# Kernel tuning notes

Hardware: AMD Instinct MI355X
Metric: run time of the kernel (lower is better)

Reference implementation:

```python
import jax, jax.numpy as jnp
import numpy as np

D, H, L, FF = 512, 8, 6, 2048
EPS = 1e-5


def _ln(x, g, b):
    m = x.mean(-1, keepdims=True)
    v = ((x - m) ** 2).mean(-1, keepdims=True)
    return (x - m) * jax.lax.rsqrt(v + EPS) * g + b


def _mha(qi, ki, vi, w, b):
    # w: [4, D, D] (q, k, v, out), b: [4, D]; weights stored [in, out]
    B, Sq, _ = qi.shape
    Sk = ki.shape[1]
    dk = D // H
    q = (qi @ w[0] + b[0]).reshape(B, Sq, H, dk)
    k = (ki @ w[1] + b[1]).reshape(B, Sk, H, dk)
    v = (vi @ w[2] + b[2]).reshape(B, Sk, H, dk)
    scores = jnp.einsum('bqhd,bkhd->bhqk', q, k) / np.float32(np.sqrt(dk))
    attn = jax.nn.softmax(scores, axis=-1)
    o = jnp.einsum('bhqk,bkhd->bqhd', attn, v).reshape(B, Sq, D)
    return o @ w[3] + b[3]


def setup_inputs() -> dict:
    key = jax.random.key(0)
    ks = jax.random.split(key, 12)
    bs, c, h, w = 4, D, 32, 32
    nq = 100
    s = np.float32(0.02)
    f32 = jnp.float32
    return {
        'src': jax.random.normal(ks[0], (bs, c, h, w), f32),
        'query_embed': jax.random.normal(ks[1], (nq, D), f32),
        'pos_embed': jax.random.normal(ks[2], (bs, c, h, w), f32),
        # encoder params (stacked over L layers)
        'enc_attn_w': jax.random.normal(ks[3], (L, 4, D, D), f32) * s,
        'enc_attn_b': jnp.zeros((L, 4, D), f32),
        'enc_w1': jax.random.normal(ks[4], (L, D, FF), f32) * s,
        'enc_b1': jnp.zeros((L, FF), f32),
        'enc_w2': jax.random.normal(ks[5], (L, FF, D), f32) * s,
        'enc_b2': jnp.zeros((L, D), f32),
        'enc_ln_w': jnp.ones((L, 2, D), f32),
        'enc_ln_b': jnp.zeros((L, 2, D), f32),
        # decoder params
        'dec_sa_w': jax.random.normal(ks[6], (L, 4, D, D), f32) * s,
        'dec_sa_b': jnp.zeros((L, 4, D), f32),
        'dec_ca_w': jax.random.normal(ks[7], (L, 4, D, D), f32) * s,
        'dec_ca_b': jnp.zeros((L, 4, D), f32),
        'dec_w1': jax.random.normal(ks[8], (L, D, FF), f32) * s,
        'dec_b1': jnp.zeros((L, FF), f32),
        'dec_w2': jax.random.normal(ks[9], (L, FF, D), f32) * s,
        'dec_b2': jnp.zeros((L, D), f32),
        'dec_ln_w': jnp.ones((L, 3, D), f32),
        'dec_ln_b': jnp.zeros((L, 3, D), f32),
    }


def reference(src, query_embed, pos_embed,
              enc_attn_w, enc_attn_b, enc_w1, enc_b1, enc_w2, enc_b2,
              enc_ln_w, enc_ln_b,
              dec_sa_w, dec_sa_b, dec_ca_w, dec_ca_b,
              dec_w1, dec_b1, dec_w2, dec_b2, dec_ln_w, dec_ln_b):
    bs, c, h, w = src.shape
    x = src.reshape(bs, c, h * w).transpose(0, 2, 1)        # [B, HW, D]
    pos = pos_embed.reshape(bs, c, h * w).transpose(0, 2, 1)  # [B, HW, D]
    qe = jnp.broadcast_to(query_embed[None], (bs,) + query_embed.shape)  # [B, NQ, D]

    def enc_step(mem, p):
        aw, ab, w1, b1, w2, b2, lnw, lnb = p
        t = mem + pos  # original re-adds pos_embed every encoder layer
        t = _ln(t + _mha(t, t, t, aw, ab), lnw[0], lnb[0])
        f = jax.nn.relu(t @ w1 + b1) @ w2 + b2
        t = _ln(t + f, lnw[1], lnb[1])
        return t, None

    memory, _ = jax.lax.scan(
        enc_step, x,
        (enc_attn_w, enc_attn_b, enc_w1, enc_b1, enc_w2, enc_b2, enc_ln_w, enc_ln_b))

    mem_in = memory + pos

    def dec_step(out, p):
        saw, sab, caw, cab, w1, b1, w2, b2, lnw, lnb = p
        t = out + qe  # original re-adds query_embed every decoder layer
        t = _ln(t + _mha(t, t, t, saw, sab), lnw[0], lnb[0])
        t = _ln(t + _mha(t, mem_in, mem_in, caw, cab), lnw[1], lnb[1])
        f = jax.nn.relu(t @ w1 + b1) @ w2 + b2
        t = _ln(t + f, lnw[2], lnb[2])
        return t, None

    tgt = jnp.zeros_like(qe)
    output, _ = jax.lax.scan(
        dec_step, tgt,
        (dec_sa_w, dec_sa_b, dec_ca_w, dec_ca_b, dec_w1, dec_b1, dec_w2, dec_b2,
         dec_ln_w, dec_ln_b))
    return output, memory
```

## Files before the change

kernel.cpp:

```cpp
#include <hip/hip_runtime.h>
#include <math.h>


typedef unsigned short bfu;
typedef unsigned int u32;
typedef __bf16 bf8v __attribute__((ext_vector_type(8)));
typedef float f32x4 __attribute__((ext_vector_type(4)));

__device__ inline bfu f2bf(float f) {
  union { float f; u32 u; } v; v.f = f;
  u32 u = v.u;
  u32 r = (u + 0x7fffu + ((u >> 16) & 1u)) >> 16;
  return (bfu)r;
}
__device__ inline float bflo(u32 u) { return __uint_as_float(u << 16); }

typedef const __attribute__((address_space(1))) u32 gas_t;
typedef __attribute__((address_space(3))) u32 las_t;
__device__ __forceinline__ void gl16(const void* g, void* l) {
  __builtin_amdgcn_global_load_lds((gas_t*)g, (las_t*)l, 16, 0, 0);
}

__global__ __launch_bounds__(256) void k_transpose(const float* __restrict__ in,
                                                   float* __restrict__ out) {
  __shared__ float tile[32][33];
  int b = blockIdx.z;
  int c0 = blockIdx.x * 32, s0 = blockIdx.y * 32;
  int tx = threadIdx.x, ty = threadIdx.y;
  for (int i = ty; i < 32; i += 8)
    tile[i][tx] = in[((size_t)(b * 512 + c0 + i)) * 1024 + s0 + tx];
  __syncthreads();
  for (int i = ty; i < 32; i += 8)
    out[((size_t)(b * 1024 + s0 + i)) * 512 + c0 + tx] = tile[tx][i];
}

__global__ __launch_bounds__(256) void k_wt(const float* __restrict__ src,
                                            bfu* __restrict__ dst,
                                            int K, int N, int nj, int lstride) {
  __shared__ bfu tile[32][33];
  int g = blockIdx.z;
  int l = g / nj, j = g - l * nj;
  const float* s = src + ((size_t)l * lstride + j) * (size_t)K * N;
  bfu* d = dst + (size_t)g * (size_t)K * N;
  int n0 = blockIdx.x * 32, k0 = blockIdx.y * 32;
  int tx = threadIdx.x, ty = threadIdx.y;
  for (int i = ty; i < 32; i += 8)
    tile[i][tx] = f2bf(s[(size_t)(k0 + i) * N + n0 + tx]);
  __syncthreads();
  for (int i = ty; i < 32; i += 8)
    d[(size_t)(n0 + i) * K + k0 + tx] = tile[tx][i];
}

__global__ void k_add_dual(const float* __restrict__ a, const float* __restrict__ b,
                           float* __restrict__ of, bfu* __restrict__ ob, int n4) {
  int i = blockIdx.x * blockDim.x + threadIdx.x;
  if (i >= n4) return;
  float4 x = ((const float4*)a)[i];
  float4 y = ((const float4*)b)[i];
  float4 r = make_float4(x.x + y.x, x.y + y.y, x.z + y.z, x.w + y.w);
  ((float4*)of)[i] = r;
  ((ushort4*)ob)[i] = make_ushort4(f2bf(r.x), f2bf(r.y), f2bf(r.z), f2bf(r.w));
}

__global__ void k_qe0(const float* __restrict__ qe, float* __restrict__ of,
                      bfu* __restrict__ ob) {
  int i = blockIdx.x * blockDim.x + threadIdx.x;
  if (i >= 51200) return;
  int row = i >> 7;
  int q = row % 100;
  int c4 = i & 127;
  float4 y = ((const float4*)qe)[q * 128 + c4];
  ((float4*)of)[i] = y;
  ((ushort4*)ob)[i] = make_ushort4(f2bf(y.x), f2bf(y.y), f2bf(y.z), f2bf(y.w));
}

__global__ __launch_bounds__(256) void k_ln_red(const float* __restrict__ A,
                                                const float* __restrict__ P,
                                                int nsplit, size_t pz,
                                                const float* __restrict__ bias,
                                                const float* __restrict__ g,
                                                const float* __restrict__ be,
                                                float* __restrict__ of,
                                                bfu* __restrict__ ob,
                                                const float* __restrict__ add2,
                                                int qe_mode,
                                                float* __restrict__ of2,
                                                bfu* __restrict__ ob2,
                                                int rows) {
  int row = blockIdx.x * 4 + (threadIdx.x >> 6);
  int lane = threadIdx.x & 63;
  if (row >= rows) return;
  const float* pa = A + (size_t)row * 512;
  float v[8];
  float s = 0.f, s2 = 0.f;
#pragma unroll
  for (int j = 0; j < 8; ++j) {
    int c = lane + j * 64;
    float x = pa[c] + bias[c];
    for (int z = 0; z < nsplit; ++z) x += P[z * pz + (size_t)row * 512 + c];
    v[j] = x; s += x; s2 += x * x;
  }
#pragma unroll
  for (int off = 32; off > 0; off >>= 1) {
    s += __shfl_xor(s, off);
    s2 += __shfl_xor(s2, off);
  }
  float mean = s * (1.f / 512.f);
  float var = s2 * (1.f / 512.f) - mean * mean;
  float r = rsqrtf(var + 1e-5f);
  int arow = qe_mode ? (row % 100) : row;
#pragma unroll
  for (int j = 0; j < 8; ++j) {
    int c = lane + j * 64;
    float o = (v[j] - mean) * r * g[c] + be[c];
    if (of) of[(size_t)row * 512 + c] = o;
    if (ob) ob[(size_t)row * 512 + c] = f2bf(o);
    if (add2) {
      float o2 = o + add2[(size_t)arow * 512 + c];
      if (of2) of2[(size_t)row * 512 + c] = o2;
      if (ob2) ob2[(size_t)row * 512 + c] = f2bf(o2);
    }
  }
}

__global__ __launch_bounds__(256) void k_gemm_bf(const bfu* __restrict__ A,
                                                 const bfu* __restrict__ Wt,
                                                 const float* __restrict__ bias,
                                                 bfu* __restrict__ C,
                                                 int M, int N, int K, int relu,
                                                 size_t wtz, size_t cz, int bz) {
  __shared__ bfu As[2][128][64];
  __shared__ bfu Bs[2][128][64];
  int z = blockIdx.z;
  Wt += (size_t)z * wtz; C += (size_t)z * cz; bias += z * bz;
  int bm = blockIdx.y * 128, bn = blockIdx.x * 128;
  int t = threadIdx.x;
  int wave = t >> 6, lane = t & 63;
  int wm = wave >> 1, wn = wave & 1;
  int l15 = lane & 15, l4 = lane >> 4;
  f32x4 acc[4][4];
  f32x4 zz = {0.f, 0.f, 0.f, 0.f};
#pragma unroll
  for (int mi = 0; mi < 4; ++mi)
#pragma unroll
    for (int ni = 0; ni < 4; ++ni) acc[mi][ni] = zz;

  auto stage = [&](int buf, int k0) {
#pragma unroll
    for (int i = 0; i < 4; ++i) {
      int c = t + i * 256;
      int row = c >> 3, kg = c & 7;
      int sc = kg ^ (row & 7);
      if (bm + row < M)
        gl16(A + (size_t)(bm + row) * K + k0 + sc * 8, &As[buf][row][kg * 8]);
      gl16(Wt + (size_t)(bn + row) * K + k0 + sc * 8, &Bs[buf][row][kg * 8]);
    }
  };
  stage(0, 0);
  int cur = 0;
  for (int k0 = 0; k0 < K; k0 += 64) {
    __syncthreads();
    if (k0 + 64 < K) stage(cur ^ 1, k0 + 64);
#pragma unroll
    for (int kc = 0; kc < 2; ++kc) {
      bf8v av[4], bv[4];
#pragma unroll
      for (int mi = 0; mi < 4; ++mi) {
        int row = wm * 64 + mi * 16 + l15;
        av[mi] = *(const bf8v*)&As[cur][row][((kc * 4 + l4) ^ (row & 7)) * 8];
      }
#pragma unroll
      for (int ni = 0; ni < 4; ++ni) {
        int row = wn * 64 + ni * 16 + l15;
        bv[ni] = *(const bf8v*)&Bs[cur][row][((kc * 4 + l4) ^ (row & 7)) * 8];
      }
#pragma unroll
      for (int mi = 0; mi < 4; ++mi)
#pragma unroll
        for (int ni = 0; ni < 4; ++ni)
          acc[mi][ni] = __builtin_amdgcn_mfma_f32_16x16x32_bf16(av[mi], bv[ni],
                                                                acc[mi][ni], 0, 0, 0);
    }
    cur ^= 1;
  }

#pragma unroll
  for (int mi = 0; mi < 4; ++mi) {
    int row0 = bm + wm * 64 + mi * 16 + l4 * 4;
#pragma unroll
    for (int ni = 0; ni < 4; ++ni) {
      int col = bn + wn * 64 + ni * 16 + l15;
      float bb = bias[col];
#pragma unroll
      for (int r = 0; r < 4; ++r) {
        int row = row0 + r;
        if (row < M) {
          float v = acc[mi][ni][r] + bb;
          if (relu) v = fmaxf(v, 0.f);
          C[(size_t)row * N + col] = f2bf(v);
        }
      }
    }
  }
}

__global__ __launch_bounds__(256) void k_gemm_sk(const bfu* __restrict__ A,
                                                 const bfu* __restrict__ Wt,
                                                 float* __restrict__ Pf,
                                                 int M, int N, int K, int ksplit) {
  __shared__ bfu As[2][128][64];
  __shared__ bfu Bs[2][128][64];
  int z = blockIdx.z;
  int Kc = K / ksplit;
  int kbeg = z * Kc;
  Pf += (size_t)z * M * N;
  int bm = blockIdx.y * 128, bn = blockIdx.x * 128;
  int t = threadIdx.x;
  int wave = t >> 6, lane = t & 63;
  int wm = wave >> 1, wn = wave & 1;
  int l15 = lane & 15, l4 = lane >> 4;
  f32x4 acc[4][4];
  f32x4 zz = {0.f, 0.f, 0.f, 0.f};
#pragma unroll
  for (int mi = 0; mi < 4; ++mi)
#pragma unroll
    for (int ni = 0; ni < 4; ++ni) acc[mi][ni] = zz;

  auto stage = [&](int buf, int k0) {
#pragma unroll
    for (int i = 0; i < 4; ++i) {
      int c = t + i * 256;
      int row = c >> 3, kg = c & 7;
      int sc = kg ^ (row & 7);
      if (bm + row < M)
        gl16(A + (size_t)(bm + row) * K + k0 + sc * 8, &As[buf][row][kg * 8]);
      gl16(Wt + (size_t)(bn + row) * K + k0 + sc * 8, &Bs[buf][row][kg * 8]);
    }
  };
  stage(0, kbeg);
  int cur = 0;
  for (int k0 = kbeg; k0 < kbeg + Kc; k0 += 64) {
    __syncthreads();
    if (k0 + 64 < kbeg + Kc) stage(cur ^ 1, k0 + 64);
#pragma unroll
    for (int kc = 0; kc < 2; ++kc) {
      bf8v av[4], bv[4];
#pragma unroll
      for (int mi = 0; mi < 4; ++mi) {
        int row = wm * 64 + mi * 16 + l15;
        av[mi] = *(const bf8v*)&As[cur][row][((kc * 4 + l4) ^ (row & 7)) * 8];
      }
#pragma unroll
      for (int ni = 0; ni < 4; ++ni) {
        int row = wn * 64 + ni * 16 + l15;
        bv[ni] = *(const bf8v*)&Bs[cur][row][((kc * 4 + l4) ^ (row & 7)) * 8];
      }
#pragma unroll
      for (int mi = 0; mi < 4; ++mi)
#pragma unroll
        for (int ni = 0; ni < 4; ++ni)
          acc[mi][ni] = __builtin_amdgcn_mfma_f32_16x16x32_bf16(av[mi], bv[ni],
                                                                acc[mi][ni], 0, 0, 0);
    }
    cur ^= 1;
  }

#pragma unroll
  for (int mi = 0; mi < 4; ++mi) {
    int row0 = bm + wm * 64 + mi * 16 + l4 * 4;
#pragma unroll
    for (int ni = 0; ni < 4; ++ni) {
      int col = bn + wn * 64 + ni * 16 + l15;
#pragma unroll
      for (int r = 0; r < 4; ++r) {
        int row = row0 + r;
        if (row < M) Pf[(size_t)row * N + col] = acc[mi][ni][r];
      }
    }
  }
}

__global__ __launch_bounds__(256) void k_attn_mfma(const bfu* __restrict__ Q, int qs,
                                                   const bfu* __restrict__ Km,
                                                   const bfu* __restrict__ Vm, int kvs,
                                                   bfu* __restrict__ O,
                                                   int Sq, int Sk) {
  __shared__ bfu Ks[128][72];
  __shared__ bfu Vt[64][136];
  __shared__ bfu Sm[4][16][136];
  const float scale = 0.125f;
  int b = blockIdx.z, h = blockIdx.y;
  int q0 = blockIdx.x * 64;
  int t = threadIdx.x;
  int wave = t >> 6, lane = t & 63;
  int l15 = lane & 15, l4 = lane >> 4;
  int hoff = h * 64;

  uint4 uq0 = {0u, 0u, 0u, 0u}, uq1 = {0u, 0u, 0u, 0u};
  {
    int qrow = q0 + wave * 16 + l15;
    if (qrow < Sq) {
      const bfu* qp = Q + (size_t)(b * Sq + qrow) * qs + hoff + l4 * 8;
      uq0 = *(const uint4*)qp;
      uq1 = *(const uint4*)(qp + 32);
    }
  }
  bf8v qf0 = *(bf8v*)&uq0, qf1 = *(bf8v*)&uq1;

  float m_[4] = {-1e30f, -1e30f, -1e30f, -1e30f};
  float l_[4] = {0.f, 0.f, 0.f, 0.f};
  f32x4 oacc[4];
  f32x4 zz = {0.f, 0.f, 0.f, 0.f};
#pragma unroll
  for (int n = 0; n < 4; ++n) oacc[n] = zz;

  uint4 ruk[4], ruv[4];
  const uint4 uz = {0u, 0u, 0u, 0u};
  auto load_kv = [&](int k0) {
#pragma unroll
    for (int i = 0; i < 4; ++i) {
      int e = t + i * 256;
      int rk = e >> 3, cg = e & 7;
      ruk[i] = uz;
      if (k0 + rk < Sk)
        ruk[i] = *(const uint4*)(Km + (size_t)(b * Sk + k0 + rk) * kvs + hoff + cg * 8);
      int kv = e & 127, dg = e >> 7;
      ruv[i] = uz;
      if (k0 + kv < Sk)
        ruv[i] = *(const uint4*)(Vm + (size_t)(b * Sk + k0 + kv) * kvs + hoff + dg * 8);
    }
  };
  load_kv(0);

  for (int k0 = 0; k0 < Sk; k0 += 128) {
#pragma unroll
    for (int i = 0; i < 4; ++i) {
      int e = t + i * 256;
      int rk = e >> 3, cg = e & 7;
      *(uint4*)&Ks[rk][cg * 8] = ruk[i];
      int kv = e & 127, dg = e >> 7;
      bfu vv[8];
      *(uint4*)vv = ruv[i];
#pragma unroll
      for (int j = 0; j < 8; ++j) Vt[dg * 8 + j][kv] = vv[j];
    }
    __syncthreads();
    if (k0 + 128 < Sk) load_kv(k0 + 128);

    f32x4 s4[8];
    __builtin_amdgcn_s_setprio(1);
#pragma unroll
    for (int tt = 0; tt < 8; ++tt) {
      bf8v kf0 = *(const bf8v*)&Ks[tt * 16 + l15][l4 * 8];
      bf8v kf1 = *(const bf8v*)&Ks[tt * 16 + l15][32 + l4 * 8];
      f32x4 a = zz;
      a = __builtin_amdgcn_mfma_f32_16x16x32_bf16(qf0, kf0, a, 0, 0, 0);
      a = __builtin_amdgcn_mfma_f32_16x16x32_bf16(qf1, kf1, a, 0, 0, 0);
      s4[tt] = a;
    }
    __builtin_amdgcn_s_setprio(0);

    float f_[4];
#pragma unroll
    for (int r = 0; r < 4; ++r) {
      float sv[8];
      float mx = -1e30f;
#pragma unroll
      for (int tt = 0; tt < 8; ++tt) {
        float s = s4[tt][r] * scale;
        s = (k0 + tt * 16 + l15 < Sk) ? s : -1e30f;
        sv[tt] = s;
        mx = fmaxf(mx, s);
      }
#pragma unroll
      for (int off = 1; off < 16; off <<= 1) mx = fmaxf(mx, __shfl_xor(mx, off));
      float nm = fmaxf(m_[r], mx);
      float f = __expf(m_[r] - nm);
      float ps = 0.f;
#pragma unroll
      for (int tt = 0; tt < 8; ++tt) {
        float p = __expf(sv[tt] - nm);
        ps += p;
        Sm[wave][l4 * 4 + r][tt * 16 + l15] = f2bf(p);
      }
#pragma unroll
      for (int off = 1; off < 16; off <<= 1) ps += __shfl_xor(ps, off);
      l_[r] = l_[r] * f + ps;
      m_[r] = nm;
      f_[r] = f;
    }
#pragma unroll
    for (int n = 0; n < 4; ++n)
#pragma unroll
      for (int r = 0; r < 4; ++r) oacc[n][r] *= f_[r];

    __builtin_amdgcn_s_setprio(1);
#pragma unroll
    for (int h2 = 0; h2 < 2; ++h2) {
      bf8v p0 = *(const bf8v*)&Sm[wave][l15][h2 * 64 + l4 * 8];
      bf8v p1 = *(const bf8v*)&Sm[wave][l15][h2 * 64 + 32 + l4 * 8];
#pragma unroll
      for (int n = 0; n < 4; ++n) {
        bf8v v0 = *(const bf8v*)&Vt[n * 16 + l15][h2 * 64 + l4 * 8];
        bf8v v1 = *(const bf8v*)&Vt[n * 16 + l15][h2 * 64 + 32 + l4 * 8];
        oacc[n] = __builtin_amdgcn_mfma_f32_16x16x32_bf16(p0, v0, oacc[n], 0, 0, 0);
        oacc[n] = __builtin_amdgcn_mfma_f32_16x16x32_bf16(p1, v1, oacc[n], 0, 0, 0);
      }
    }
    __builtin_amdgcn_s_setprio(0);
    __syncthreads();
  }

#pragma unroll
  for (int r = 0; r < 4; ++r) {
    int row = q0 + wave * 16 + l4 * 4 + r;
    if (row < Sq) {
      float inv = 1.f / l_[r];
#pragma unroll
      for (int n = 0; n < 4; ++n)
        O[(size_t)(b * Sq + row) * 512 + hoff + n * 16 + l15] = f2bf(oacc[n][r] * inv);
    }
  }
}


extern "C" void kernel_launch(void* const* d_in, const int* in_sizes, int n_in,
                              void* d_out, int out_size, void* d_ws, size_t ws_size,
                              hipStream_t stream) {
  const float* src         = (const float*)d_in[0];
  const float* query_embed = (const float*)d_in[1];
  const float* pos_embed   = (const float*)d_in[2];
  const float* enc_attn_w  = (const float*)d_in[3];
  const float* enc_attn_b  = (const float*)d_in[4];
  const float* enc_w1      = (const float*)d_in[5];
  const float* enc_b1      = (const float*)d_in[6];
  const float* enc_w2      = (const float*)d_in[7];
  const float* enc_b2      = (const float*)d_in[8];
  const float* enc_ln_w    = (const float*)d_in[9];
  const float* enc_ln_b    = (const float*)d_in[10];
  const float* dec_sa_w    = (const float*)d_in[11];
  const float* dec_sa_b    = (const float*)d_in[12];
  const float* dec_ca_w    = (const float*)d_in[13];
  const float* dec_ca_b    = (const float*)d_in[14];
  const float* dec_w1      = (const float*)d_in[15];
  const float* dec_b1      = (const float*)d_in[16];
  const float* dec_w2      = (const float*)d_in[17];
  const float* dec_b2      = (const float*)d_in[18];
  const float* dec_ln_w    = (const float*)d_in[19];
  const float* dec_ln_b    = (const float*)d_in[20];
  float* out = (float*)d_out;

  const size_t ENC = 4UL * 1024 * 512;
  const size_t DEC = 4UL * 100 * 512;
  const size_t MAT = 512UL * 512;

  float* p = (float*)d_ws;
  float* x    = p; p += ENC;
  float* pos  = p; p += ENC;
  float* t1   = p; p += ENC;
  float* t2   = p; p += ENC;
  float* t3   = p; p += DEC;
  float* Pf   = p; p += 4 * ENC;

  bfu* bp = (bfu*)p;
  bfu* t1b    = bp; bp += ENC;
  bfu* t2b    = bp; bp += ENC;
  bfu* t3b    = bp; bp += DEC;
  bfu* qkvb   = bp; bp += 4096UL * 1536;
  bfu* aob    = bp; bp += ENC;
  bfu* hbb    = bp; bp += 4096UL * 2048;
  bfu* meminb = bp; bp += ENC;
  bfu* ckvb   = bp; bp += 6UL * 4096 * 1024;
  bfu* enc_qkv_t = bp; bp += 18 * MAT;
  bfu* enc_out_t = bp; bp += 6 * MAT;
  bfu* enc_w1t   = bp; bp += 6UL * 512 * 2048;
  bfu* enc_w2t   = bp; bp += 6UL * 2048 * 512;
  bfu* dsa_qkv_t = bp; bp += 18 * MAT;
  bfu* dsa_out_t = bp; bp += 6 * MAT;
  bfu* dca_q_t   = bp; bp += 6 * MAT;
  bfu* dca_kv_t  = bp; bp += 12 * MAT;
  bfu* dca_out_t = bp; bp += 6 * MAT;
  bfu* dw1t      = bp; bp += 6UL * 512 * 2048;
  bfu* dw2t      = bp; bp += 6UL * 2048 * 512;

  dim3 tb(32, 8);
  k_transpose<<<dim3(16, 32, 4), tb, 0, stream>>>(src, x);
  k_transpose<<<dim3(16, 32, 4), tb, 0, stream>>>(pos_embed, pos);

  k_wt<<<dim3(16, 16, 18), tb, 0, stream>>>(enc_attn_w,            enc_qkv_t, 512, 512, 3, 4);
  k_wt<<<dim3(16, 16, 6),  tb, 0, stream>>>(enc_attn_w + 3 * MAT,  enc_out_t, 512, 512, 1, 4);
  k_wt<<<dim3(64, 16, 6),  tb, 0, stream>>>(enc_w1,                enc_w1t,   512, 2048, 1, 1);
  k_wt<<<dim3(16, 64, 6),  tb, 0, stream>>>(enc_w2,                enc_w2t,   2048, 512, 1, 1);
  k_wt<<<dim3(16, 16, 18), tb, 0, stream>>>(dec_sa_w,              dsa_qkv_t, 512, 512, 3, 4);
  k_wt<<<dim3(16, 16, 6),  tb, 0, stream>>>(dec_sa_w + 3 * MAT,    dsa_out_t, 512, 512, 1, 4);
  k_wt<<<dim3(16, 16, 6),  tb, 0, stream>>>(dec_ca_w,              dca_q_t,   512, 512, 1, 4);
  k_wt<<<dim3(16, 16, 12), tb, 0, stream>>>(dec_ca_w + 1 * MAT,    dca_kv_t,  512, 512, 2, 4);
  k_wt<<<dim3(16, 16, 6),  tb, 0, stream>>>(dec_ca_w + 3 * MAT,    dca_out_t, 512, 512, 1, 4);
  k_wt<<<dim3(64, 16, 6),  tb, 0, stream>>>(dec_w1,                dw1t,      512, 2048, 1, 1);
  k_wt<<<dim3(16, 64, 6),  tb, 0, stream>>>(dec_w2,                dw2t,      2048, 512, 1, 1);

  k_add_dual<<<2048, 256, 0, stream>>>(x, pos, t1, t1b, (int)(ENC / 4));
  for (int l = 0; l < 6; ++l) {
    const float* ab = enc_attn_b + (size_t)l * 2048;
    k_gemm_bf<<<dim3(12, 32), 256, 0, stream>>>(t1b, enc_qkv_t + (size_t)l * 3 * MAT, ab,
                                                qkvb, 4096, 1536, 512, 0, 0, 0, 0);
    k_attn_mfma<<<dim3(16, 8, 4), 256, 0, stream>>>(qkvb, 1536, qkvb + 512, qkvb + 1024, 1536,
                                                    aob, 1024, 1024);
    k_gemm_sk<<<dim3(4, 32, 2), 256, 0, stream>>>(aob, enc_out_t + (size_t)l * MAT, Pf,
                                                  4096, 512, 512, 2);
    k_ln_red<<<1024, 256, 0, stream>>>(t1, Pf, 2, ENC, ab + 1536,
                                       enc_ln_w + (size_t)(l * 2 + 0) * 512,
                                       enc_ln_b + (size_t)(l * 2 + 0) * 512,
                                       t2, t2b, (const float*)nullptr, 0,
                                       (float*)nullptr, (bfu*)nullptr, 4096);
    k_gemm_bf<<<dim3(16, 32), 256, 0, stream>>>(t2b, enc_w1t + (size_t)l * 512 * 2048,
                                                enc_b1 + (size_t)l * 2048, hbb,
                                                4096, 2048, 512, 1, 0, 0, 0);
    k_gemm_sk<<<dim3(4, 32, 4), 256, 0, stream>>>(hbb, enc_w2t + (size_t)l * 2048 * 512, Pf,
                                                  4096, 512, 2048, 4);
    if (l < 5) {
      k_ln_red<<<1024, 256, 0, stream>>>(t2, Pf, 4, ENC, enc_b2 + (size_t)l * 512,
                                         enc_ln_w + (size_t)(l * 2 + 1) * 512,
                                         enc_ln_b + (size_t)(l * 2 + 1) * 512,
                                         (float*)nullptr, (bfu*)nullptr,
                                         pos, 0, t1, t1b, 4096);
    } else {
      k_ln_red<<<1024, 256, 0, stream>>>(t2, Pf, 4, ENC, enc_b2 + (size_t)l * 512,
                                         enc_ln_w + (size_t)(l * 2 + 1) * 512,
                                         enc_ln_b + (size_t)(l * 2 + 1) * 512,
                                         out + DEC, (bfu*)nullptr,
                                         pos, 0, (float*)nullptr, meminb, 4096);
    }
  }

  k_gemm_bf<<<dim3(8, 32, 6), 256, 0, stream>>>(meminb, dca_kv_t, dec_ca_b + 512,
                                                ckvb, 4096, 1024, 512, 0,
                                                2 * MAT, 4096UL * 1024, 2048);

  k_qe0<<<200, 256, 0, stream>>>(query_embed, t1, t1b);
  for (int l = 0; l < 6; ++l) {
    const float* sb = dec_sa_b + (size_t)l * 2048;
    const float* cb = dec_ca_b + (size_t)l * 2048;
    k_gemm_bf<<<dim3(12, 4), 256, 0, stream>>>(t1b, dsa_qkv_t + (size_t)l * 3 * MAT, sb,
                                               qkvb, 400, 1536, 512, 0, 0, 0, 0);
    k_attn_mfma<<<dim3(2, 8, 4), 256, 0, stream>>>(qkvb, 1536, qkvb + 512, qkvb + 1024, 1536,
                                                   aob, 100, 100);
    k_gemm_sk<<<dim3(4, 4, 2), 256, 0, stream>>>(aob, dsa_out_t + (size_t)l * MAT, Pf,
                                                 400, 512, 512, 2);
    k_ln_red<<<100, 256, 0, stream>>>(t1, Pf, 2, 400UL * 512, sb + 1536,
                                      dec_ln_w + (size_t)(l * 3 + 0) * 512,
                                      dec_ln_b + (size_t)(l * 3 + 0) * 512,
                                      t2, t2b, (const float*)nullptr, 0,
                                      (float*)nullptr, (bfu*)nullptr, 400);
    k_gemm_bf<<<dim3(4, 4), 256, 0, stream>>>(t2b, dca_q_t + (size_t)l * MAT, cb,
                                              qkvb, 400, 512, 512, 0, 0, 0, 0);
    k_attn_mfma<<<dim3(2, 8, 4), 256, 0, stream>>>(qkvb, 512,
                                                   ckvb + (size_t)l * 4096 * 1024,
                                                   ckvb + (size_t)l * 4096 * 1024 + 512, 1024,
                                                   aob, 100, 1024);
    k_gemm_sk<<<dim3(4, 4, 2), 256, 0, stream>>>(aob, dca_out_t + (size_t)l * MAT, Pf,
                                                 400, 512, 512, 2);
    k_ln_red<<<100, 256, 0, stream>>>(t2, Pf, 2, 400UL * 512, cb + 1536,
                                      dec_ln_w + (size_t)(l * 3 + 1) * 512,
                                      dec_ln_b + (size_t)(l * 3 + 1) * 512,
                                      t3, t3b, (const float*)nullptr, 0,
                                      (float*)nullptr, (bfu*)nullptr, 400);
    k_gemm_bf<<<dim3(16, 4), 256, 0, stream>>>(t3b, dw1t + (size_t)l * 512 * 2048,
                                               dec_b1 + (size_t)l * 2048, hbb,
                                               400, 2048, 512, 1, 0, 0, 0);
    k_gemm_sk<<<dim3(4, 4, 4), 256, 0, stream>>>(hbb, dw2t + (size_t)l * 2048 * 512, Pf,
                                                 400, 512, 2048, 4);
    if (l < 5) {
      k_ln_red<<<100, 256, 0, stream>>>(t3, Pf, 4, 400UL * 512, dec_b2 + (size_t)l * 512,
                                        dec_ln_w + (size_t)(l * 3 + 2) * 512,
                                        dec_ln_b + (size_t)(l * 3 + 2) * 512,
                                        (float*)nullptr, (bfu*)nullptr,
                                        query_embed, 1, t1, t1b, 400);
    } else {
      k_ln_red<<<100, 256, 0, stream>>>(t3, Pf, 4, 400UL * 512, dec_b2 + (size_t)l * 512,
                                        dec_ln_w + (size_t)(l * 3 + 2) * 512,
                                        dec_ln_b + (size_t)(l * 3 + 2) * 512,
                                        out, (bfu*)nullptr,
                                        (const float*)nullptr, 0,
                                        (float*)nullptr, (bfu*)nullptr, 400);
    }
  }
}
```

Baseline: 1.997 ms.

## Fuse output-projection and FFN2 GEMMs with residual LayerNorm epilogue

Replaces the split-K GEMM plus separate LayerNorm reduction kernels with a single GEMM kernel that computes full 512-wide rows per block (32 rows x 512 cols) and applies bias, residual add, and LayerNorm in the epilogue through a cross-wave shared-memory reduction. This drops the fp32 partial-sum buffer and its write/read traffic, and removes one kernel launch per sublayer. Weight transposes are merged into fewer launches and the two input transposes into one. The trade-off is far fewer blocks (128 for the encoder, 13 for the decoder) with no split-K, so the decoder GEMMs, especially the K=2048 FFN2, run on very few CUs.

Result: slower. 2.615 ms (+31.0%).

```diff
diff --git a/kernel.cpp b/kernel.cpp
--- a/kernel.cpp
+++ b/kernel.cpp
@@ -21,26 +21,30 @@
   __builtin_amdgcn_global_load_lds((gas_t*)g, (las_t*)l, 16, 0, 0);
 }
 
-__global__ __launch_bounds__(256) void k_transpose(const float* __restrict__ in,
-                                                   float* __restrict__ out) {
+__global__ __launch_bounds__(256) void k_transpose2(const float* __restrict__ s0,
+                                                    const float* __restrict__ s1,
+                                                    float* __restrict__ d0,
+                                                    float* __restrict__ d1) {
   __shared__ float tile[32][33];
-  int b = blockIdx.z;
-  int c0 = blockIdx.x * 32, s0 = blockIdx.y * 32;
+  int zz = blockIdx.z;
+  const float* in = (zz < 4) ? s0 : s1;
+  float* out = (zz < 4) ? d0 : d1;
+  int b = zz & 3;
+  int c0 = blockIdx.x * 32, s0i = blockIdx.y * 32;
   int tx = threadIdx.x, ty = threadIdx.y;
   for (int i = ty; i < 32; i += 8)
-    tile[i][tx] = in[((size_t)(b * 512 + c0 + i)) * 1024 + s0 + tx];
+    tile[i][tx] = in[((size_t)(b * 512 + c0 + i)) * 1024 + s0i + tx];
   __syncthreads();
   for (int i = ty; i < 32; i += 8)
-    out[((size_t)(b * 1024 + s0 + i)) * 512 + c0 + tx] = tile[tx][i];
+    out[((size_t)(b * 1024 + s0i + i)) * 512 + c0 + tx] = tile[tx][i];
 }
 
 __global__ __launch_bounds__(256) void k_wt(const float* __restrict__ src,
                                             bfu* __restrict__ dst,
-                                            int K, int N, int nj, int lstride) {
+                                            int K, int N) {
   __shared__ bfu tile[32][33];
   int g = blockIdx.z;
-  int l = g / nj, j = g - l * nj;
-  const float* s = src + ((size_t)l * lstride + j) * (size_t)K * N;
+  const float* s = src + (size_t)g * (size_t)K * N;
   bfu* d = dst + (size_t)g * (size_t)K * N;
   int n0 = blockIdx.x * 32, k0 = blockIdx.y * 32;
   int tx = threadIdx.x, ty = threadIdx.y;
@@ -72,55 +76,6 @@
   float4 y = ((const float4*)qe)[q * 128 + c4];
   ((float4*)of)[i] = y;
   ((ushort4*)ob)[i] = make_ushort4(f2bf(y.x), f2bf(y.y), f2bf(y.z), f2bf(y.w));
-}
-
-__global__ __launch_bounds__(256) void k_ln_red(const float* __restrict__ A,
-                                                const float* __restrict__ P,
-                                                int nsplit, size_t pz,
-                                                const float* __restrict__ bias,
-                                                const float* __restrict__ g,
-                                                const float* __restrict__ be,
-                                                float* __restrict__ of,
-                                                bfu* __restrict__ ob,
-                                                const float* __restrict__ add2,
-                                                int qe_mode,
-                                                float* __restrict__ of2,
-                                                bfu* __restrict__ ob2,
-                                                int rows) {
-  int row = blockIdx.x * 4 + (threadIdx.x >> 6);
-  int lane = threadIdx.x & 63;
-  if (row >= rows) return;
-  const float* pa = A + (size_t)row * 512;
-  float v[8];
-  float s = 0.f, s2 = 0.f;
-#pragma unroll
-  for (int j = 0; j < 8; ++j) {
-    int c = lane + j * 64;
-    float x = pa[c] + bias[c];
-    for (int z = 0; z < nsplit; ++z) x += P[z * pz + (size_t)row * 512 + c];
-    v[j] = x; s += x; s2 += x * x;
-  }
-#pragma unroll
-  for (int off = 32; off > 0; off >>= 1) {
-    s += __shfl_xor(s, off);
-    s2 += __shfl_xor(s2, off);
-  }
-  float mean = s * (1.f / 512.f);
-  float var = s2 * (1.f / 512.f) - mean * mean;
-  float r = rsqrtf(var + 1e-5f);
-  int arow = qe_mode ? (row % 100) : row;
-#pragma unroll
-  for (int j = 0; j < 8; ++j) {
-    int c = lane + j * 64;
-    float o = (v[j] - mean) * r * g[c] + be[c];
-    if (of) of[(size_t)row * 512 + c] = o;
-    if (ob) ob[(size_t)row * 512 + c] = f2bf(o);
-    if (add2) {
-      float o2 = o + add2[(size_t)arow * 512 + c];
-      if (of2) of2[(size_t)row * 512 + c] = o2;
-      if (ob2) ob2[(size_t)row * 512 + c] = f2bf(o2);
-    }
-  }
 }
 
 __global__ __launch_bounds__(256) void k_gemm_bf(const bfu* __restrict__ A,
@@ -204,80 +159,125 @@
   }
 }
 
-__global__ __launch_bounds__(256) void k_gemm_sk(const bfu* __restrict__ A,
+__global__ __launch_bounds__(256) void k_gemm_ln(const bfu* __restrict__ A,
                                                  const bfu* __restrict__ Wt,
-                                                 float* __restrict__ Pf,
-                                                 int M, int N, int K, int ksplit) {
-  __shared__ bfu As[2][128][64];
-  __shared__ bfu Bs[2][128][64];
-  int z = blockIdx.z;
-  int Kc = K / ksplit;
-  int kbeg = z * Kc;
-  Pf += (size_t)z * M * N;
-  int bm = blockIdx.y * 128, bn = blockIdx.x * 128;
+                                                 const float* __restrict__ bias,
+                                                 const float* __restrict__ R,
+                                                 const float* __restrict__ g,
+                                                 const float* __restrict__ be,
+                                                 float* __restrict__ of,
+                                                 bfu* __restrict__ ob,
+                                                 const float* __restrict__ add2,
+                                                 int qe_mode,
+                                                 float* __restrict__ of2,
+                                                 bfu* __restrict__ ob2,
+                                                 int M, int K) {
+  __shared__ bfu As[2][32][32];
+  __shared__ bfu Bs[2][512][32];
+  __shared__ float red[32][4][2];
+  int bm = blockIdx.x * 32;
   int t = threadIdx.x;
   int wave = t >> 6, lane = t & 63;
-  int wm = wave >> 1, wn = wave & 1;
   int l15 = lane & 15, l4 = lane >> 4;
-  f32x4 acc[4][4];
+  f32x4 acc[2][8];
   f32x4 zz = {0.f, 0.f, 0.f, 0.f};
 #pragma unroll
-  for (int mi = 0; mi < 4; ++mi)
-#pragma unroll
-    for (int ni = 0; ni < 4; ++ni) acc[mi][ni] = zz;
+  for (int mt = 0; mt < 2; ++mt)
+#pragma unroll
+    for (int nt = 0; nt < 8; ++nt) acc[mt][nt] = zz;
 
   auto stage = [&](int buf, int k0) {
 #pragma unroll
-    for (int i = 0; i < 4; ++i) {
-      int c = t + i * 256;
-      int row = c >> 3, kg = c & 7;
-      int sc = kg ^ (row & 7);
-      if (bm + row < M)
-        gl16(A + (size_t)(bm + row) * K + k0 + sc * 8, &As[buf][row][kg * 8]);
-      gl16(Wt + (size_t)(bn + row) * K + k0 + sc * 8, &Bs[buf][row][kg * 8]);
+    for (int i = 0; i < 8; ++i) {
+      int cb = t + i * 256;
+      int r = cb >> 2, p = cb & 3;
+      int gp = p ^ ((r >> 2) & 3);
+      gl16(Wt + (size_t)r * K + k0 + gp * 8, &Bs[buf][r][p * 8]);
+    }
+    if (t < 128) {
+      int r = t >> 2, p = t & 3;
+      int gp = p ^ ((r >> 2) & 3);
+      if (bm + r < M)
+        gl16(A + (size_t)(bm + r) * K + k0 + gp * 8, &As[buf][r][p * 8]);
     }
   };
-  stage(0, kbeg);
+  stage(0, 0);
   int cur = 0;
-  for (int k0 = kbeg; k0 < kbeg + Kc; k0 += 64) {
+  for (int k0 = 0; k0 < K; k0 += 32) {
     __syncthreads();
-    if (k0 + 64 < kbeg + Kc) stage(cur ^ 1, k0 + 64);
-#pragma unroll
-    for (int kc = 0; kc < 2; ++kc) {
-      bf8v av[4], bv[4];
-#pragma unroll
-      for (int mi = 0; mi < 4; ++mi) {
-        int row = wm * 64 + mi * 16 + l15;
-        av[mi] = *(const bf8v*)&As[cur][row][((kc * 4 + l4) ^ (row & 7)) * 8];
-      }
-#pragma unroll
-      for (int ni = 0; ni < 4; ++ni) {
-        int row = wn * 64 + ni * 16 + l15;
-        bv[ni] = *(const bf8v*)&Bs[cur][row][((kc * 4 + l4) ^ (row & 7)) * 8];
-      }
-#pragma unroll
-      for (int mi = 0; mi < 4; ++mi)
-#pragma unroll
-        for (int ni = 0; ni < 4; ++ni)
-          acc[mi][ni] = __builtin_amdgcn_mfma_f32_16x16x32_bf16(av[mi], bv[ni],
-                                                                acc[mi][ni], 0, 0, 0);
+    if (k0 + 32 < K) stage(cur ^ 1, k0 + 32);
+    bf8v av[2];
+#pragma unroll
+    for (int mt = 0; mt < 2; ++mt) {
+      int r = mt * 16 + l15;
+      av[mt] = *(const bf8v*)&As[cur][r][(l4 ^ ((r >> 2) & 3)) * 8];
+    }
+#pragma unroll
+    for (int nt = 0; nt < 8; ++nt) {
+      int rb = wave * 128 + nt * 16 + l15;
+      bf8v bv = *(const bf8v*)&Bs[cur][rb][(l4 ^ ((rb >> 2) & 3)) * 8];
+      acc[0][nt] = __builtin_amdgcn_mfma_f32_16x16x32_bf16(av[0], bv, acc[0][nt], 0, 0, 0);
+      acc[1][nt] = __builtin_amdgcn_mfma_f32_16x16x32_bf16(av[1], bv, acc[1][nt], 0, 0, 0);
     }
     cur ^= 1;
   }
 
-#pragma unroll
-  for (int mi = 0; mi < 4; ++mi) {
-    int row0 = bm + wm * 64 + mi * 16 + l4 * 4;
-#pragma unroll
-    for (int ni = 0; ni < 4; ++ni) {
-      int col = bn + wn * 64 + ni * 16 + l15;
-#pragma unroll
-      for (int r = 0; r < 4; ++r) {
-        int row = row0 + r;
-        if (row < M) Pf[(size_t)row * N + col] = acc[mi][ni][r];
-      }
-    }
-  }
+  float bs[8], gg[8], bb[8];
+#pragma unroll
+  for (int nt = 0; nt < 8; ++nt) {
+    int gc = wave * 128 + nt * 16 + l15;
+    bs[nt] = bias[gc]; gg[nt] = g[gc]; bb[nt] = be[gc];
+  }
+#pragma unroll
+  for (int mt = 0; mt < 2; ++mt)
+#pragma unroll
+    for (int rr = 0; rr < 4; ++rr) {
+      int row32 = mt * 16 + l4 * 4 + rr;
+      int gm = bm + row32;
+      float s = 0.f, s2 = 0.f;
+      if (gm < M) {
+#pragma unroll
+        for (int nt = 0; nt < 8; ++nt) {
+          int gc = wave * 128 + nt * 16 + l15;
+          float v = acc[mt][nt][rr] + bs[nt] + R[(size_t)gm * 512 + gc];
+          acc[mt][nt][rr] = v;
+          s += v; s2 += v * v;
+        }
+      }
+#pragma unroll
+      for (int off = 1; off < 16; off <<= 1) {
+        s += __shfl_xor(s, off);
+        s2 += __shfl_xor(s2, off);
+      }
+      if (l15 == 0) { red[row32][wave][0] = s; red[row32][wave][1] = s2; }
+    }
+  __syncthreads();
+#pragma unroll
+  for (int mt = 0; mt < 2; ++mt)
+#pragma unroll
+    for (int rr = 0; rr < 4; ++rr) {
+      int row32 = mt * 16 + l4 * 4 + rr;
+      int gm = bm + row32;
+      if (gm >= M) continue;
+      float s = red[row32][0][0] + red[row32][1][0] + red[row32][2][0] + red[row32][3][0];
+      float s2 = red[row32][0][1] + red[row32][1][1] + red[row32][2][1] + red[row32][3][1];
+      float mean = s * (1.f / 512.f);
+      float var = s2 * (1.f / 512.f) - mean * mean;
+      float rs = rsqrtf(var + 1e-5f);
+      int arow = qe_mode ? (gm % 100) : gm;
+#pragma unroll
+      for (int nt = 0; nt < 8; ++nt) {
+        int gc = wave * 128 + nt * 16 + l15;
+        float o = (acc[mt][nt][rr] - mean) * rs * gg[nt] + bb[nt];
+        if (of) of[(size_t)gm * 512 + gc] = o;
+        if (ob) ob[(size_t)gm * 512 + gc] = f2bf(o);
+        if (add2) {
+          float o2 = o + add2[(size_t)arow * 512 + gc];
+          if (of2) of2[(size_t)gm * 512 + gc] = o2;
+          if (ob2) ob2[(size_t)gm * 512 + gc] = f2bf(o2);
+        }
+      }
+    }
 }
 
 __global__ __launch_bounds__(256) void k_attn_mfma(const bfu* __restrict__ Q, int qs,
@@ -460,7 +460,6 @@
   float* t1   = p; p += ENC;
   float* t2   = p; p += ENC;
   float* t3   = p; p += DEC;
-  float* Pf   = p; p += 4 * ENC;
 
   bfu* bp = (bfu*)p;
   bfu* t1b    = bp; bp += ENC;
@@ -471,118 +470,106 @@
   bfu* hbb    = bp; bp += 4096UL * 2048;
   bfu* meminb = bp; bp += ENC;
   bfu* ckvb   = bp; bp += 6UL * 4096 * 1024;
-  bfu* enc_qkv_t = bp; bp += 18 * MAT;
-  bfu* enc_out_t = bp; bp += 6 * MAT;
+  bfu* enc_att_t = bp; bp += 24 * MAT;
   bfu* enc_w1t   = bp; bp += 6UL * 512 * 2048;
   bfu* enc_w2t   = bp; bp += 6UL * 2048 * 512;
-  bfu* dsa_qkv_t = bp; bp += 18 * MAT;
-  bfu* dsa_out_t = bp; bp += 6 * MAT;
-  bfu* dca_q_t   = bp; bp += 6 * MAT;
-  bfu* dca_kv_t  = bp; bp += 12 * MAT;
-  bfu* dca_out_t = bp; bp += 6 * MAT;
+  bfu* dsa_t     = bp; bp += 24 * MAT;
+  bfu* dca_t     = bp; bp += 24 * MAT;
   bfu* dw1t      = bp; bp += 6UL * 512 * 2048;
   bfu* dw2t      = bp; bp += 6UL * 2048 * 512;
 
   dim3 tb(32, 8);
-  k_transpose<<<dim3(16, 32, 4), tb, 0, stream>>>(src, x);
-  k_transpose<<<dim3(16, 32, 4), tb, 0, stream>>>(pos_embed, pos);
-
-  k_wt<<<dim3(16, 16, 18), tb, 0, stream>>>(enc_attn_w,            enc_qkv_t, 512, 512, 3, 4);
-  k_wt<<<dim3(16, 16, 6),  tb, 0, stream>>>(enc_attn_w + 3 * MAT,  enc_out_t, 512, 512, 1, 4);
-  k_wt<<<dim3(64, 16, 6),  tb, 0, stream>>>(enc_w1,                enc_w1t,   512, 2048, 1, 1);
-  k_wt<<<dim3(16, 64, 6),  tb, 0, stream>>>(enc_w2,                enc_w2t,   2048, 512, 1, 1);
-  k_wt<<<dim3(16, 16, 18), tb, 0, stream>>>(dec_sa_w,              dsa_qkv_t, 512, 512, 3, 4);
-  k_wt<<<dim3(16, 16, 6),  tb, 0, stream>>>(dec_sa_w + 3 * MAT,    dsa_out_t, 512, 512, 1, 4);
-  k_wt<<<dim3(16, 16, 6),  tb, 0, stream>>>(dec_ca_w,              dca_q_t,   512, 512, 1, 4);
-  k_wt<<<dim3(16, 16, 12), tb, 0, stream>>>(dec_ca_w + 1 * MAT,    dca_kv_t,  512, 512, 2, 4);
-  k_wt<<<dim3(16, 16, 6),  tb, 0, stream>>>(dec_ca_w + 3 * MAT,    dca_out_t, 512, 512, 1, 4);
-  k_wt<<<dim3(64, 16, 6),  tb, 0, stream>>>(dec_w1,                dw1t,      512, 2048, 1, 1);
-  k_wt<<<dim3(16, 64, 6),  tb, 0, stream>>>(dec_w2,                dw2t,      2048, 512, 1, 1);
+  k_transpose2<<<dim3(16, 32, 8), tb, 0, stream>>>(src, pos_embed, x, pos);
+
+  k_wt<<<dim3(16, 16, 24), tb, 0, stream>>>(enc_attn_w, enc_att_t, 512, 512);
+  k_wt<<<dim3(64, 16, 6),  tb, 0, stream>>>(enc_w1,     enc_w1t,   512, 2048);
+  k_wt<<<dim3(16, 64, 6),  tb, 0, stream>>>(enc_w2,     enc_w2t,   2048, 512);
+  k_wt<<<dim3(16, 16, 24), tb, 0, stream>>>(dec_sa_w,   dsa_t,     512, 512);
+  k_wt<<<dim3(16, 16, 24), tb, 0, stream>>>(dec_ca_w,   dca_t,     512, 512);
+  k_wt<<<dim3(64, 16, 6),  tb, 0, stream>>>(dec_w1,     dw1t,      512, 2048);
+  k_wt<<<dim3(16, 64, 6),  tb, 0, stream>>>(dec_w2,     dw2t,      2048, 512);
 
   k_add_dual<<<2048, 256, 0, stream>>>(x, pos, t1, t1b, (int)(ENC / 4));
   for (int l = 0; l < 6; ++l) {
+    const bfu* awt = enc_att_t + (size_t)l * 4 * MAT;
     const float* ab = enc_attn_b + (size_t)l * 2048;
-    k_gemm_bf<<<dim3(12, 32), 256, 0, stream>>>(t1b, enc_qkv_t + (size_t)l * 3 * MAT, ab,
+    k_gemm_bf<<<dim3(12, 32), 256, 0, stream>>>(t1b, awt, ab,
                                                 qkvb, 4096, 1536, 512, 0, 0, 0, 0);
     k_attn_mfma<<<dim3(16, 8, 4), 256, 0, stream>>>(qkvb, 1536, qkvb + 512, qkvb + 1024, 1536,
                                                     aob, 1024, 1024);
-    k_gemm_sk<<<dim3(4, 32, 2), 256, 0, stream>>>(aob, enc_out_t + (size_t)l * MAT, Pf,
-                                                  4096, 512, 512, 2);
-    k_ln_red<<<1024, 256, 0, stream>>>(t1, Pf, 2, ENC, ab + 1536,
+    k_gemm_ln<<<128, 256, 0, stream>>>(aob, awt + 3 * MAT, ab + 1536, t1,
                                        enc_ln_w + (size_t)(l * 2 + 0) * 512,
                                        enc_ln_b + (size_t)(l * 2 + 0) * 512,
                                        t2, t2b, (const float*)nullptr, 0,
-                                       (float*)nullptr, (bfu*)nullptr, 4096);
+                                       (float*)nullptr, (bfu*)nullptr, 4096, 512);
     k_gemm_bf<<<dim3(16, 32), 256, 0, stream>>>(t2b, enc_w1t + (size_t)l * 512 * 2048,
                                                 enc_b1 + (size_t)l * 2048, hbb,
                                                 4096, 2048, 512, 1, 0, 0, 0);
-    k_gemm_sk<<<dim3(4, 32, 4), 256, 0, stream>>>(hbb, enc_w2t + (size_t)l * 2048 * 512, Pf,
-                                                  4096, 512, 2048, 4);
     if (l < 5) {
-      k_ln_red<<<1024, 256, 0, stream>>>(t2, Pf, 4, ENC, enc_b2 + (size_t)l * 512,
+      k_gemm_ln<<<128, 256, 0, stream>>>(hbb, enc_w2t + (size_t)l * 2048 * 512,
+                                         enc_b2 + (size_t)l * 512, t2,
                                          enc_ln_w + (size_t)(l * 2 + 1) * 512,
                                          enc_ln_b + (size_t)(l * 2 + 1) * 512,
                                          (float*)nullptr, (bfu*)nullptr,
-                                         pos, 0, t1, t1b, 4096);
+                                         pos, 0, t1, t1b, 4096, 2048);
     } else {
-      k_ln_red<<<1024, 256, 0, stream>>>(t2, Pf, 4, ENC, enc_b2 + (size_t)l * 512,
+      k_gemm_ln<<<128, 256, 0, stream>>>(hbb, enc_w2t + (size_t)l * 2048 * 512,
+                                         enc_b2 + (size_t)l * 512, t2,
                                          enc_ln_w + (size_t)(l * 2 + 1) * 512,
                                          enc_ln_b + (size_t)(l * 2 + 1) * 512,
                                          out + DEC, (bfu*)nullptr,
-                                         pos, 0, (float*)nullptr, meminb, 4096);
-    }
-  }
-
-  k_gemm_bf<<<dim3(8, 32, 6), 256, 0, stream>>>(meminb, dca_kv_t, dec_ca_b + 512,
+                                         pos, 0, (float*)nullptr, meminb, 4096, 2048);
+    }
+  }
+
+  k_gemm_bf<<<dim3(8, 32, 6), 256, 0, stream>>>(meminb, dca_t + MAT, dec_ca_b + 512,
                                                 ckvb, 4096, 1024, 512, 0,
-                                                2 * MAT, 4096UL * 1024, 2048);
+                                                4 * MAT, 4096UL * 1024, 2048);
 
   k_qe0<<<200, 256, 0, stream>>>(query_embed, t1, t1b);
   for (int l = 0; l < 6; ++l) {
+    const bfu* swt = dsa_t + (size_t)l * 4 * MAT;
+    const bfu* cwt = dca_t + (size_t)l * 4 * MAT;
     const float* sb = dec_sa_b + (size_t)l * 2048;
     const float* cb = dec_ca_b + (size_t)l * 2048;
-    k_gemm_bf<<<dim3(12, 4), 256, 0, stream>>>(t1b, dsa_qkv_t + (size_t)l * 3 * MAT, sb,
+    k_gemm_bf<<<dim3(12, 4), 256, 0, stream>>>(t1b, swt, sb,
                                                qkvb, 400, 1536, 512, 0, 0, 0, 0);
     k_attn_mfma<<<dim3(2, 8, 4), 256, 0, stream>>>(qkvb, 1536, qkvb + 512, qkvb + 1024, 1536,
                                                    aob, 100, 100);
-    k_gemm_sk<<<dim3(4, 4, 2), 256, 0, stream>>>(aob, dsa_out_t + (size_t)l * MAT, Pf,
-                                                 400, 512, 512, 2);
-    k_ln_red<<<100, 256, 0, stream>>>(t1, Pf, 2, 400UL * 512, sb + 1536,
+    k_gemm_ln<<<13, 256, 0, stream>>>(aob, swt + 3 * MAT, sb + 1536, t1,
                                       dec_ln_w + (size_t)(l * 3 + 0) * 512,
                                       dec_ln_b + (size_t)(l * 3 + 0) * 512,
                                       t2, t2b, (const float*)nullptr, 0,
-                                      (float*)nullptr, (bfu*)nullptr, 400);
-    k_gemm_bf<<<dim3(4, 4), 256, 0, stream>>>(t2b, dca_q_t + (size_t)l * MAT, cb,
+                                      (float*)nullptr, (bfu*)nullptr, 400, 512);
+    k_gemm_bf<<<dim3(4, 4), 256, 0, stream>>>(t2b, cwt, cb,
                                               qkvb, 400, 512, 512, 0, 0, 0, 0);
     k_attn_mfma<<<dim3(2, 8, 4), 256, 0, stream>>>(qkvb, 512,
                                                    ckvb + (size_t)l * 4096 * 1024,
                                                    ckvb + (size_t)l * 4096 * 1024 + 512, 1024,
                                                    aob, 100, 1024);
-    k_gemm_sk<<<dim3(4, 4, 2), 256, 0, stream>>>(aob, dca_out_t + (size_t)l * MAT, Pf,
-                                                 400, 512, 512, 2);
-    k_ln_red<<<100, 256, 0, stream>>>(t2, Pf, 2, 400UL * 512, cb + 1536,
+    k_gemm_ln<<<13, 256, 0, stream>>>(aob, cwt + 3 * MAT, cb + 1536, t2,
                                       dec_ln_w + (size_t)(l * 3 + 1) * 512,
                                       dec_ln_b + (size_t)(l * 3 + 1) * 512,
                                       t3, t3b, (const float*)nullptr, 0,
-                                      (float*)nullptr, (bfu*)nullptr, 400);
+                                      (float*)nullptr, (bfu*)nullptr, 400, 512);
     k_gemm_bf<<<dim3(16, 4), 256, 0, stream>>>(t3b, dw1t + (size_t)l * 512 * 2048,
                                                dec_b1 + (size_t)l * 2048, hbb,
                                                400, 2048, 512, 1, 0, 0, 0);
-    k_gemm_sk<<<dim3(4, 4, 4), 256, 0, stream>>>(hbb, dw2t + (size_t)l * 2048 * 512, Pf,
-                                                 400, 512, 2048, 4);
     if (l < 5) {
-      k_ln_red<<<100, 256, 0, stream>>>(t3, Pf, 4, 400UL * 512, dec_b2 + (size_t)l * 512,
+      k_gemm_ln<<<13, 256, 0, stream>>>(hbb, dw2t + (size_t)l * 2048 * 512,
+                                        dec_b2 + (size_t)l * 512, t3,
                                         dec_ln_w + (size_t)(l * 3 + 2) * 512,
                                         dec_ln_b + (size_t)(l * 3 + 2) * 512,
                                         (float*)nullptr, (bfu*)nullptr,
-                                        query_embed, 1, t1, t1b, 400);
+                                        query_embed, 1, t1, t1b, 400, 2048);
     } else {
-      k_ln_red<<<100, 256, 0, stream>>>(t3, Pf, 4, 400UL * 512, dec_b2 + (size_t)l * 512,
+      k_gemm_ln<<<13, 256, 0, stream>>>(hbb, dw2t + (size_t)l * 2048 * 512,
+                                        dec_b2 + (size_t)l * 512, t3,
                                         dec_ln_w + (size_t)(l * 3 + 2) * 512,
                                         dec_ln_b + (size_t)(l * 3 + 2) * 512,
                                         out, (bfu*)nullptr,
                                         (const float*)nullptr, 0,
-                                        (float*)nullptr, (bfu*)nullptr, 400);
-    }
-  }
-}
+                                        (float*)nullptr, (bfu*)nullptr, 400, 2048);
+    }
+  }
+}
```
